# Kernel tuning notes

Hardware: AMD Instinct MI355X
Metric: run time of the kernel (lower is better)

Reference implementation:

```python
import jax, jax.numpy as jnp
import numpy as np

B, H, S, DH = 2, 16, 2048, 64

def setup_inputs() -> dict:
    key = jax.random.key(0)
    k1, k2, k3 = jax.random.split(key, 3)
    return {
        "query": jax.random.normal(k1, (B, H, S, DH), dtype=jnp.float32),
        "key": jax.random.normal(k2, (B, H, S, DH), dtype=jnp.float32),
        "value": jax.random.normal(k3, (B, H, S, DH), dtype=jnp.float32),
        "key_padding_mask": jnp.zeros((B, S), dtype=bool),
    }

def reference(query, key, value, key_padding_mask):
    # scores: [B, H, Sq, Sk]
    scale = 1.0 / jnp.sqrt(jnp.asarray(query.shape[-1], query.dtype))
    scores = jnp.einsum("bhqd,bhkd->bhqk", query, key) * scale
    # key padding mask broadcasts over heads and query positions
    scores = jnp.where(key_padding_mask[:, None, None, :], -jnp.inf, scores)
    attn = jax.nn.softmax(scores, axis=-1)
    # dropout is identity in eval mode (deterministic reference)
    out = jnp.einsum("bhqk,bhkd->bhqd", attn, value)
    # [B, H, S, Dh] -> [B, S, H*Dh]
    b, h, s, dh = out.shape
    return out.transpose(0, 2, 1, 3).reshape(b, s, h * dh)
```

## Files before the change

kernel.cpp:

```cpp
#include <hip/hip_runtime.h>

typedef __attribute__((ext_vector_type(4))) float f32x4;
typedef __attribute__((ext_vector_type(4))) short s16x4;
typedef __attribute__((ext_vector_type(8))) short s16x8;

constexpr int Bn = 2, Hn = 16, Sn = 2048, DHn = 64;
constexpr int TQ = 64;
constexpr int TK = 64;
constexpr int NT = Sn / TK;
constexpr int TILE_SH = TK * DHn;
constexpr float SHIFT = 16.0f;

__device__ __forceinline__ unsigned pk2(float a, float b) {
  unsigned ua = __builtin_bit_cast(unsigned, a);
  unsigned ub = __builtin_bit_cast(unsigned, b);
  ua += 0x7fffu + ((ua >> 16) & 1u);
  ub += 0x7fffu + ((ub >> 16) & 1u);
  return (ua >> 16) | (ub & 0xffff0000u);
}

__device__ __forceinline__ float fexp2(float x) {
#if __has_builtin(__builtin_amdgcn_exp2f)
  return __builtin_amdgcn_exp2f(x);
#else
  return exp2f(x);
#endif
}

__device__ __forceinline__ void gl2lds16(const short* g, short* l) {
  __builtin_amdgcn_global_load_lds(
      (const __attribute__((address_space(1))) void*)g,
      (__attribute__((address_space(3))) void*)l, 16, 0, 0);
}

__global__ __launch_bounds__(256)
void prepack_kernel(const float* __restrict__ Kg, const float* __restrict__ Vg,
                    short* __restrict__ Kp, short* __restrict__ Vp) {
  const int blk = blockIdx.x;
  const int tid = threadIdx.x;
  const float* Kt = Kg + (size_t)blk * TILE_SH;
  const float* Vt = Vg + (size_t)blk * TILE_SH;
  short* Kd = Kp + (size_t)blk * TILE_SH;
  short* Vd = Vp + (size_t)blk * TILE_SH;

  {
    const int r = tid >> 2;
    const int cb = (tid & 3) * 2;
#pragma unroll
    for (int cc = 0; cc < 2; ++cc) {
      int c = cb + cc;
      const float4* p = (const float4*)(Kt + (size_t)r * DHn + c * 8);
      float4 x = p[0], y = p[1];
      union { unsigned u[4]; s16x8 v; } tmp;
      tmp.u[0] = pk2(x.x, x.y); tmp.u[1] = pk2(x.z, x.w);
      tmp.u[2] = pk2(y.x, y.y); tmp.u[3] = pk2(y.z, y.w);
      *(s16x8*)&Kd[r * 64 + (c ^ (r & 7)) * 8] = tmp.v;
    }
  }
  {
    const int d = tid & 63;
    const int kb = (tid >> 6) * 16;
#pragma unroll
    for (int cc = 0; cc < 2; ++cc) {
      int k0 = kb + cc * 8;
      float v0[8];
#pragma unroll
      for (int j = 0; j < 8; ++j) v0[j] = Vt[(size_t)(k0 + j) * DHn + d];
      union { unsigned u[4]; s16x8 v; } tmp;
      tmp.u[0] = pk2(v0[0], v0[1]); tmp.u[1] = pk2(v0[2], v0[3]);
      tmp.u[2] = pk2(v0[4], v0[5]); tmp.u[3] = pk2(v0[6], v0[7]);
      int c = k0 >> 3;
      *(s16x8*)&Vd[d * 64 + (c ^ (d & 7)) * 8] = tmp.v;
    }
  }
}

__global__ __launch_bounds__(256, 4)
void fattn_kernel(const float* __restrict__ Qg, const short* __restrict__ Kp,
                  const short* __restrict__ Vp, const unsigned char* __restrict__ maskg,
                  float* __restrict__ Og) {
  __shared__ __align__(16) short Ksh[TILE_SH];
  __shared__ __align__(16) short VTsh[TILE_SH];
  __shared__ __align__(16) short Psh[4 * 16 * 64];

  const int tid  = threadIdx.x;
  const int w    = tid >> 6;
  const int lane = tid & 63;
  const int n    = lane & 15;
  const int q4   = lane >> 4;
  const int swz  = n & 7;

  const int blk = blockIdx.x;
  const int bh  = blk & 31;
  const int qt  = blk >> 5;
  const int b   = bh >> 4;
  const int h   = bh & 15;

  const float* Qb = Qg + (size_t)bh * Sn * DHn;
  const short* Kt = Kp + (size_t)bh * NT * TILE_SH;
  const short* Vt = Vp + (size_t)bh * NT * TILE_SH;
  const unsigned char* mq = maskg + (size_t)b * Sn;

  const int q0 = qt * TQ + w * 16;

  const float c1 = 0.125f * 1.4426950408889634f;
  s16x8 qf[2];
  {
    const float* qrow = Qb + (size_t)(q0 + n) * DHn;
#pragma unroll
    for (int kc = 0; kc < 2; ++kc) {
      const float4* p = (const float4*)(qrow + kc * 32 + q4 * 8);
      float4 x = p[0], y = p[1];
      union { unsigned u[4]; s16x8 v; } tmp;
      tmp.u[0] = pk2(x.x * c1, x.y * c1);
      tmp.u[1] = pk2(x.z * c1, x.w * c1);
      tmp.u[2] = pk2(y.x * c1, y.y * c1);
      tmp.u[3] = pk2(y.z * c1, y.w * c1);
      qf[kc] = tmp.v;
    }
  }

  const int c0   = q4 ^ swz;
  const int offA = n * 64 + c0 * 8;
  const int offB = n * 64 + (c0 ^ 4) * 8;
  const int prow = (w * 16 + n) * 64;
  const int pc   = (q4 >> 1) ^ swz;
  const int pwo  = (q4 & 1) * 4;

  f32x4 Oa[4];
#pragma unroll
  for (int na = 0; na < 4; ++na) Oa[na] = (f32x4){0.f, 0.f, 0.f, 0.f};
  float lsum = 0.f;

  unsigned m4[4];
#pragma unroll
  for (int mc = 0; mc < 4; ++mc)
    m4[mc] = *(const unsigned*)&mq[mc * 16 + q4 * 4];

  for (int t = 0; t < NT; ++t) {
    __syncthreads();

    {
      const short* Kg2 = Kt + (size_t)t * TILE_SH;
      const short* Vg2 = Vt + (size_t)t * TILE_SH;
#pragma unroll
      for (int k = 0; k < 2; ++k) {
        gl2lds16(Kg2 + k * 2048 + tid * 8, &Ksh[k * 2048 + w * 512]);
        gl2lds16(Vg2 + k * 2048 + tid * 8, &VTsh[k * 2048 + w * 512]);
      }
    }

    f32x4 bias[4];
#pragma unroll
    for (int mc = 0; mc < 4; ++mc)
#pragma unroll
      for (int r = 0; r < 4; ++r)
        bias[mc][r] = ((m4[mc] >> (8 * r)) & 0xffu) ? -1e30f : -SHIFT;

    if (t + 1 < NT) {
#pragma unroll
      for (int mc = 0; mc < 4; ++mc)
        m4[mc] = *(const unsigned*)&mq[(t + 1) * TK + mc * 16 + q4 * 4];
    }

    __syncthreads();

    s16x8 kf[4][2];
#pragma unroll
    for (int mc = 0; mc < 4; ++mc) {
      kf[mc][0] = *(const s16x8*)&Ksh[mc * 1024 + offA];
      kf[mc][1] = *(const s16x8*)&Ksh[mc * 1024 + offB];
    }

    f32x4 sa[4];
#pragma unroll
    for (int mc = 0; mc < 4; ++mc) sa[mc] = bias[mc];
    __builtin_amdgcn_s_setprio(1);
#pragma unroll
    for (int mc = 0; mc < 4; ++mc)
#pragma unroll
      for (int kc = 0; kc < 2; ++kc)
        sa[mc] = __builtin_amdgcn_mfma_f32_16x16x32_bf16(kf[mc][kc], qf[kc], sa[mc], 0, 0, 0);
    __builtin_amdgcn_s_setprio(0);

    float ls = 0.f;
#pragma unroll
    for (int mc = 0; mc < 4; ++mc) {
      float p0 = fexp2(sa[mc][0]);
      float p1 = fexp2(sa[mc][1]);
      float p2 = fexp2(sa[mc][2]);
      float p3 = fexp2(sa[mc][3]);
      ls += (p0 + p1) + (p2 + p3);
      union { unsigned u[2]; s16x4 v4; } pw;
      pw.u[0] = pk2(p0, p1);
      pw.u[1] = pk2(p2, p3);
      *(s16x4*)&Psh[prow + ((pc ^ (2 * mc)) * 8) + pwo] = pw.v4;
    }
    lsum += ls;

    s16x8 vf[4][2];
#pragma unroll
    for (int na = 0; na < 4; ++na) {
      vf[na][0] = *(const s16x8*)&VTsh[na * 1024 + offA];
      vf[na][1] = *(const s16x8*)&VTsh[na * 1024 + offB];
    }
    s16x8 pf[2];
    pf[0] = *(const s16x8*)&Psh[prow + ((q4 ^ swz) * 8)];
    pf[1] = *(const s16x8*)&Psh[prow + (((4 + q4) ^ swz) * 8)];
    __builtin_amdgcn_s_setprio(1);
#pragma unroll
    for (int na = 0; na < 4; ++na)
#pragma unroll
      for (int kc = 0; kc < 2; ++kc)
        Oa[na] = __builtin_amdgcn_mfma_f32_16x16x32_bf16(pf[kc], vf[na][kc], Oa[na], 0, 0, 0);
    __builtin_amdgcn_s_setprio(0);
  }

  lsum += __shfl_xor(lsum, 16);
  lsum += __shfl_xor(lsum, 32);
#pragma unroll
  for (int r = 0; r < 4; ++r) {
    float lr  = __shfl(lsum, q4 * 4 + r);
    float inv = 1.0f / lr;
    int q = q0 + q4 * 4 + r;
    float* orow = Og + (size_t)(b * Sn + q) * (Hn * DHn) + h * DHn;
#pragma unroll
    for (int na = 0; na < 4; ++na)
      orow[na * 16 + n] = Oa[na][r] * inv;
  }
}

extern "C" void kernel_launch(void* const* d_in, const int* in_sizes, int n_in,
                              void* d_out, int out_size, void* d_ws, size_t ws_size,
                              hipStream_t stream) {
  (void)in_sizes; (void)n_in; (void)ws_size; (void)out_size;
  const float* Q = (const float*)d_in[0];
  const float* K = (const float*)d_in[1];
  const float* V = (const float*)d_in[2];
  const unsigned char* mask = (const unsigned char*)d_in[3];
  float* out = (float*)d_out;

  short* Kp = (short*)d_ws;
  short* Vp = Kp + (size_t)Bn * Hn * Sn * DHn;

  hipLaunchKernelGGL(prepack_kernel, dim3(Bn * Hn * NT), dim3(256), 0, stream, K, V, Kp, Vp);
  hipLaunchKernelGGL(fattn_kernel, dim3(Bn * Hn * (Sn / TQ)), dim3(256), 0, stream,
                     Q, Kp, Vp, mask, out);
}
```

Measured before the change: 156.6 us.

## Double-buffer K/V tiles in LDS with two-ahead async prefetch

Splits the K and V shared-memory tiles into two buffers. The kernel preloads the first two tiles, then at the end of each iteration issues the async global-to-LDS load for tile t+2 into the buffer it just finished with. Completion is tracked with manual s_waitcnt vmcnt and s_barrier in place of the two __syncthreads per tile, so global load latency can overlap the MFMA and softmax work. In exchange, LDS per block roughly doubles, which may limit occupancy. The final iterations also issue redundant clamped loads, and correctness depends on vmcnt ordering, including the interleaved mask loads.

```diff
diff --git a/kernel.cpp b/kernel.cpp
--- a/kernel.cpp
+++ b/kernel.cpp
@@ -79,8 +79,8 @@
 void fattn_kernel(const float* __restrict__ Qg, const short* __restrict__ Kp,
                   const short* __restrict__ Vp, const unsigned char* __restrict__ maskg,
                   float* __restrict__ Og) {
-  __shared__ __align__(16) short Ksh[TILE_SH];
-  __shared__ __align__(16) short VTsh[TILE_SH];
+  __shared__ __align__(16) short Ksh[2][TILE_SH];
+  __shared__ __align__(16) short VTsh[2][TILE_SH];
   __shared__ __align__(16) short Psh[4 * 16 * 64];
 
   const int tid  = threadIdx.x;
@@ -137,18 +137,20 @@
   for (int mc = 0; mc < 4; ++mc)
     m4[mc] = *(const unsigned*)&mq[mc * 16 + q4 * 4];
 
+#pragma unroll
+  for (int k = 0; k < 2; ++k) {
+    gl2lds16(Kt + k * 2048 + tid * 8, &Ksh[0][k * 2048 + w * 512]);
+    gl2lds16(Vt + k * 2048 + tid * 8, &VTsh[0][k * 2048 + w * 512]);
+  }
+#pragma unroll
+  for (int k = 0; k < 2; ++k) {
+    gl2lds16(Kt + TILE_SH + k * 2048 + tid * 8, &Ksh[1][k * 2048 + w * 512]);
+    gl2lds16(Vt + TILE_SH + k * 2048 + tid * 8, &VTsh[1][k * 2048 + w * 512]);
+  }
+  asm volatile("s_waitcnt vmcnt(4)\n\ts_barrier" ::: "memory");
+
   for (int t = 0; t < NT; ++t) {
-    __syncthreads();
-
-    {
-      const short* Kg2 = Kt + (size_t)t * TILE_SH;
-      const short* Vg2 = Vt + (size_t)t * TILE_SH;
-#pragma unroll
-      for (int k = 0; k < 2; ++k) {
-        gl2lds16(Kg2 + k * 2048 + tid * 8, &Ksh[k * 2048 + w * 512]);
-        gl2lds16(Vg2 + k * 2048 + tid * 8, &VTsh[k * 2048 + w * 512]);
-      }
-    }
+    const int cur = t & 1;
 
     f32x4 bias[4];
 #pragma unroll
@@ -157,19 +159,18 @@
       for (int r = 0; r < 4; ++r)
         bias[mc][r] = ((m4[mc] >> (8 * r)) & 0xffu) ? -1e30f : -SHIFT;
 
-    if (t + 1 < NT) {
+    {
+      const int tn = (t + 1 < NT) ? t + 1 : NT - 1;
 #pragma unroll
       for (int mc = 0; mc < 4; ++mc)
-        m4[mc] = *(const unsigned*)&mq[(t + 1) * TK + mc * 16 + q4 * 4];
-    }
-
-    __syncthreads();
+        m4[mc] = *(const unsigned*)&mq[tn * TK + mc * 16 + q4 * 4];
+    }
 
     s16x8 kf[4][2];
 #pragma unroll
     for (int mc = 0; mc < 4; ++mc) {
-      kf[mc][0] = *(const s16x8*)&Ksh[mc * 1024 + offA];
-      kf[mc][1] = *(const s16x8*)&Ksh[mc * 1024 + offB];
+      kf[mc][0] = *(const s16x8*)&Ksh[cur][mc * 1024 + offA];
+      kf[mc][1] = *(const s16x8*)&Ksh[cur][mc * 1024 + offB];
     }
 
     f32x4 sa[4];
@@ -201,8 +202,8 @@
     s16x8 vf[4][2];
 #pragma unroll
     for (int na = 0; na < 4; ++na) {
-      vf[na][0] = *(const s16x8*)&VTsh[na * 1024 + offA];
-      vf[na][1] = *(const s16x8*)&VTsh[na * 1024 + offB];
+      vf[na][0] = *(const s16x8*)&VTsh[cur][na * 1024 + offA];
+      vf[na][1] = *(const s16x8*)&VTsh[cur][na * 1024 + offB];
     }
     s16x8 pf[2];
     pf[0] = *(const s16x8*)&Psh[prow + ((q4 ^ swz) * 8)];
@@ -214,6 +215,21 @@
       for (int kc = 0; kc < 2; ++kc)
         Oa[na] = __builtin_amdgcn_mfma_f32_16x16x32_bf16(pf[kc], vf[na][kc], Oa[na], 0, 0, 0);
     __builtin_amdgcn_s_setprio(0);
+
+    asm volatile("s_waitcnt lgkmcnt(0)\n\ts_barrier" ::: "memory");
+
+    {
+      const int ts = (t + 2 < NT) ? t + 2 : NT - 1;
+      const short* Kg2 = Kt + (size_t)ts * TILE_SH;
+      const short* Vg2 = Vt + (size_t)ts * TILE_SH;
+#pragma unroll
+      for (int k = 0; k < 2; ++k) {
+        gl2lds16(Kg2 + k * 2048 + tid * 8, &Ksh[cur][k * 2048 + w * 512]);
+        gl2lds16(Vg2 + k * 2048 + tid * 8, &VTsh[cur][k * 2048 + w * 512]);
+      }
+    }
+
+    asm volatile("s_waitcnt vmcnt(8)\n\ts_barrier" ::: "memory");
   }
 
   lsum += __shfl_xor(lsum, 16);
```

Measured after the change: 155.5 us. Within noise of the previous version (-0.7%).
